# Optimization experiments

Hardware: AMD Instinct MI355X
Metric: run time of the kernel (lower is better)

The kernel has to match this reference:

```python
import jax, jax.numpy as jnp
import numpy as np
import math

EPS = 1e-7
LMAX = 2
SPH = (LMAX + 1) ** 2  # 9
NUM_RBF = 64
CUTOFF = 6.0
N_NODES = 10000
N_EDGES = 100000
CH = 64
HID = 128
ENV_P = 5  # polynomial envelope exponent


def _small_d(l, beta):
    # complex Wigner small-d matrix d^l(beta)
    n = 2 * l + 1
    d = np.zeros((n, n))
    f = math.factorial
    c = math.cos(beta / 2.0)
    s = math.sin(beta / 2.0)
    for mp in range(-l, l + 1):
        for m in range(-l, l + 1):
            val = 0.0
            for k in range(max(0, m - mp), min(l + m, l - mp) + 1):
                val += ((-1.0) ** (mp - m + k)
                        * math.sqrt(f(l + mp) * f(l - mp) * f(l + m) * f(l - m))
                        / (f(l + m - k) * f(k) * f(mp - m + k) * f(l - mp - k))
                        * c ** (2 * l + m - mp - 2 * k) * s ** (mp - m + 2 * k))
            d[mp + l, m + l] = val
    return d


def _real_J(l):
    # real-basis Wigner d at beta=pi/2 (the 'Jd' matrices)
    d = _small_d(l, math.pi / 2.0).astype(np.complex128)
    n = 2 * l + 1
    C = np.zeros((n, n), dtype=np.complex128)
    for m in range(-l, l + 1):
        if m == 0:
            C[l, l] = 1.0
        elif m > 0:
            C[m + l, -m + l] = 1.0 / math.sqrt(2)
            C[m + l, m + l] = (-1) ** m / math.sqrt(2)
        else:
            C[m + l, m + l] = 1j / math.sqrt(2)
            C[m + l, -m + l] = -1j * (-1) ** m / math.sqrt(2)
    return np.real(C @ d @ C.conj().T)


JD_LIST = [jnp.asarray(_real_J(l), dtype=jnp.float32) for l in range(LMAX + 1)]


def _z_rot_mat(angle, l):
    # real z-rotation representation of degree l, batched over edges
    E = angle.shape[0]
    size = 2 * l + 1
    M = jnp.zeros((E, size, size), dtype=angle.dtype)
    for i in range(size):
        freq = l - i
        M = M.at[:, i, i].set(jnp.cos(freq * angle))
        M = M.at[:, i, size - 1 - i].set(jnp.sin(freq * angle))
    return M


def wigner_D(l, alpha, beta, gamma, Jd):
    Xa = _z_rot_mat(alpha, l)
    Xb = _z_rot_mat(beta, l)
    Xc = _z_rot_mat(gamma, l)
    r = jnp.einsum('bij,jk->bik', Xa, Jd)
    r = jnp.einsum('bij,bjk->bik', r, Xb)
    r = jnp.einsum('bij,jk->bik', r, Jd)
    return jnp.einsum('bij,bjk->bik', r, Xc)


def eulers_to_wigner(eulers, start_lmax, end_lmax):
    alpha, beta, gamma = eulers
    E = alpha.shape[0]
    size = (end_lmax + 1) ** 2 - start_lmax ** 2
    W = jnp.zeros((E, size, size), dtype=alpha.dtype)
    start = 0
    for l in range(start_lmax, end_lmax + 1):
        blk = wigner_D(l, alpha, beta, gamma, JD_LIST[l])
        end = start + 2 * l + 1
        W = W.at[:, start:end, start:end].set(blk)
        start = end
    return W


def init_edge_rot_euler_angles(edge_distance_vec):
    norm = jnp.linalg.norm(edge_distance_vec, axis=-1, keepdims=True)
    xyz = edge_distance_vec / jnp.maximum(norm, EPS)
    xyz = jnp.clip(xyz, -1.0, 1.0)
    x, y, z = xyz[:, 0], xyz[:, 1], xyz[:, 2]
    beta = jnp.arccos(jnp.clip(y, -1 + EPS, 1 - EPS))
    alpha = jnp.arctan2(x, z)
    gamma = jnp.zeros_like(alpha)
    return (-gamma, -beta, -alpha)


def setup_inputs() -> dict:
    key = jax.random.key(0)
    ks = jax.random.split(key, 8)
    node_feats = jax.random.normal(ks[0], (N_NODES, SPH, CH), dtype=jnp.float32)
    edge_distance_vec = jax.random.normal(ks[1], (N_EDGES, 3), dtype=jnp.float32)
    edge_index = jax.random.randint(ks[2], (2, N_EDGES), 0, N_NODES, dtype=jnp.int32)
    W_rad1 = jax.random.normal(ks[3], (NUM_RBF, HID), dtype=jnp.float32) / np.sqrt(NUM_RBF)
    b_rad1 = jnp.zeros((HID,), dtype=jnp.float32)
    W_rad2 = jax.random.normal(ks[4], (HID, CH), dtype=jnp.float32) / np.sqrt(HID)
    W_msg1 = jax.random.normal(ks[5], (CH, CH), dtype=jnp.float32) / np.sqrt(CH)
    W_msg2 = jax.random.normal(ks[6], (CH, CH), dtype=jnp.float32) / np.sqrt(CH)
    gamma = jnp.ones((CH,), dtype=jnp.float32)
    return {"node_feats": node_feats, "edge_distance_vec": edge_distance_vec,
            "edge_index": edge_index, "W_rad1": W_rad1, "b_rad1": b_rad1,
            "W_rad2": W_rad2, "W_msg1": W_msg1, "W_msg2": W_msg2, "gamma": gamma}


def reference(node_feats, edge_distance_vec, edge_index, W_rad1, b_rad1, W_rad2, W_msg1, W_msg2, gamma):
    src, dst = edge_index[0], edge_index[1]
    # per-edge block-diagonal Wigner rotation [E, SPH, SPH]
    wig = eulers_to_wigner(init_edge_rot_euler_angles(edge_distance_vec), 0, LMAX)
    # radial basis (Gaussian smearing) + polynomial envelope + MLP
    dist = jnp.linalg.norm(edge_distance_vec, axis=-1)
    offsets = jnp.linspace(0.0, CUTOFF, NUM_RBF)
    coeff = -0.5 / (offsets[1] - offsets[0]) ** 2
    rbf = jnp.exp(coeff * (dist[:, None] - offsets[None, :]) ** 2)  # [E, NUM_RBF]
    d = dist / CUTOFF
    p = ENV_P
    env = (1.0 - (p + 1) * (p + 2) / 2.0 * d ** p + p * (p + 2) * d ** (p + 1)
           - p * (p + 1) / 2.0 * d ** (p + 2))
    env = jnp.where(d < 1.0, env, 0.0)
    rad = jax.nn.silu(rbf @ W_rad1 + b_rad1) @ W_rad2  # [E, CH]
    rad = rad * env[:, None]
    # gather -> rotate -> channel mix * radial gate -> mix -> rotate back
    x = node_feats[src]                                   # [E, SPH, CH]
    x = jnp.einsum('eij,ejc->eic', wig, x)
    x = jnp.einsum('eic,cd->eid', x, W_msg1) * rad[:, None, :]
    x = jnp.einsum('eic,cd->eid', x, W_msg2)
    x = jnp.einsum('eji,ejc->eic', wig, x)                # inverse (transpose) rotation
    # scatter-reduce to destination nodes
    out = jax.ops.segment_sum(x, dst, num_segments=N_NODES)  # [N, SPH, CH]
    # equivariant RMS norm over spherical-harmonic coefficients per channel
    rms = jnp.sqrt(jnp.mean(out ** 2, axis=1, keepdims=True) + EPS)
    return out / rms * gamma[None, None, :]
```

## Files before the change

### kernel.cpp

```cpp
#include <hip/hip_runtime.h>

#define SPHN 9
#define CHN 64
#define TABLE_N 8193
#define TABLE_DT (6.0f / 8192.0f)
#define TABLE_INV_DT (8192.0f / 6.0f)

__device__ __forceinline__ void centry(int l, int r, int c, double& re, double& im)
{
    const double is2 = 0.70710678118654752440;
    re = 0.0; im = 0.0;
    int m = r - l;
    if (m == 0) {
        if (c == l) re = 1.0;
    } else if (m > 0) {
        if (c == l - m) re = is2;
        else if (c == l + m) re = (m & 1) ? -is2 : is2;
    } else {
        if (c == l + m) im = is2;
        else if (c == l - m) im = (m & 1) ? is2 : -is2;
    }
}

__global__ __launch_bounds__(256) void k_setup(float* __restrict__ Jout,
// ... 42 lines not shown
        const int n1 = n - 1;
        double jr = 0.0;
        double cjr, cji, ckr, cki;
        {
            int k = i;
            centry(l, j, j, cjr, cji);
            double tr = dS[base + k * n + j] * cjr;
            double ti = -dS[base + k * n + j] * cji;
            if (n1 - j != j) {
                centry(l, j, n1 - j, cjr, cji);
                tr += dS[base + k * n + (n1 - j)] * cjr;
                ti += -dS[base + k * n + (n1 - j)] * cji;
            }
            centry(l, i, i, ckr, cki);
            jr += ckr * tr - cki * ti;
        }
        if (n1 - i != i) {
            int k = n1 - i;
            centry(l, j, j, cjr, cji);
            double tr = dS[base + k * n + j] * cjr;
            double ti = -dS[base + k * n + j] * cji;
            if (n1 - j != j) {
                centry(l, j, n1 - j, cjr, cji);
                tr += dS[base + k * n + (n1 - j)] * cjr;
                ti += -dS[base + k * n + (n1 - j)] * cji;
            }
            centry(l, i, n1 - i, ckr, cki);
            jr += ckr * tr - cki * ti;
        }
        Jout[base + i * n + j] = (float)jr;
    }
}

__global__ __launch_bounds__(256) void k_xm(const float* __restrict__ nf,
                                            const float* __restrict__ m1,
                                            float* __restrict__ xm6, int N)
{
    const int tid = threadIdx.x;
    const int w = tid >> 6;
    const int t = tid & 63;
    const int n = blockIdx.x * 4 + w;
    __shared__ float sx[4][6 * 64];
    if (n < N) {
        const float* xp = nf + (size_t)n * (SPHN * CHN);
        sx[w][0 * 64 + t] = xp[1 * 64 + t];
        sx[w][1 * 64 + t] = xp[3 * 64 + t];
        sx[w][2 * 64 + t] = xp[4 * 64 + t];
        sx[w][3 * 64 + t] = xp[5 * 64 + t];
        sx[w][4 * 64 + t] = xp[7 * 64 + t];
        sx[w][5 * 64 + t] = xp[8 * 64 + t];
    }
    __syncthreads();
    if (n >= N) return;
    float a0 = 0.f, a1 = 0.f, a2 = 0.f, a3 = 0.f, a4 = 0.f, a5 = 0.f;
    for (int c = 0; c < 64; ++c) {
        float m = m1[c * 64 + t];
        a0 += sx[w][0 * 64 + c] * m;
        a1 += sx[w][1 * 64 + c] * m;
        a2 += sx[w][2 * 64 + c] * m;
        a3 += sx[w][3 * 64 + c] * m;
        a4 += sx[w][4 * 64 + c] * m;
        a5 += sx[w][5 * 64 + c] * m;
    }
    float* op = xm6 + (size_t)n * 384;
    op[0 * 64 + t] = a0;
    op[1 * 64 + t] = a1;
    op[2 * 64 + t] = a2;
    op[3 * 64 + t] = a3;
    op[4 * 64 + t] = a4;
    op[5 * 64 + t] = a5;
}

__device__ __forceinline__ float siluf(float x) { return x / (1.f + expf(-x)); }

__global__ __launch_bounds__(256) void k_hist(const int* __restrict__ eidx,
                                              int* __restrict__ counts, int E)
{
    int e = blockIdx.x * 256 + threadIdx.x;
    if (e < E) atomicAdd(&counts[eidx[E + e]], 1);
}

__global__ __launch_bounds__(1024) void k_scan(const int* __restrict__ counts,
                                               int* __restrict__ offsets,
                                               int* __restrict__ cursors, int N)
{
    __shared__ int wsum[16];
    __shared__ int wpre[16];
    const int tid = threadIdx.x;
    const int lane = tid & 63;
    const int wid = tid >> 6;
    const int per = (N + 1023) >> 10;
    const int begin = tid * per;
    const int endi = (begin + per < N) ? (begin + per) : N;

    int s = 0;
    for (int i = begin; i < endi; ++i) s += counts[i];

    int inc = s;
#pragma unroll
    for (int off = 1; off < 64; off <<= 1) {
        int u = __shfl_up(inc, off, 64);
        if (lane >= off) inc += u;
    }
    if (lane == 63) wsum[wid] = inc;
    __syncthreads();
    if (wid == 0) {
        int v = (lane < 16) ? wsum[lane] : 0;
        int winc = v;
#pragma unroll
        for (int off = 1; off < 16; off <<= 1) {
            int u = __shfl_up(winc, off, 64);
            if (lane >= off) winc += u;
        }
        if (lane < 16) wpre[lane] = winc - v;
    }
    __syncthreads();
    int run = wpre[wid] + (inc - s);
    for (int i = begin; i < endi; ++i) {
        int c = counts[i];
        offsets[i] = run;
        cursors[i] = run;
        run += c;
    }
    if (endi == N && begin < N) offsets[N] = run;
}

__global__ __launch_bounds__(256) void k_scatter(const int* __restrict__ eidx,
                                                 int* __restrict__ cursors,
                                                 int* __restrict__ perm,
                                                 int* __restrict__ srcs, int E)
{
    int e = blockIdx.x * 256 + threadIdx.x;
    if (e < E) {
        int pos = atomicAdd(&cursors[eidx[E + e]], 1);
        perm[pos] = e;
        srcs[pos] = eidx[e];
    }
}

__global__ __launch_bounds__(256) void k_radtab(const float* __restrict__ w1,
                                                const float* __restrict__ b1,
                                                const float* __restrict__ w2,
                                                float* __restrict__ table)
{
    __shared__ float rbfT[64 * 64];
    __shared__ float hT[128 * 64];
    __shared__ float distS[64];
    __shared__ float envS[64];
    const int tid = threadIdx.x;
    const int base = blockIdx.x * 64;

    if (tid < 64) {
        float dist = (float)(base + tid) * TABLE_DT;
        distS[tid] = dist;
        float dd = dist * (1.0f / 6.0f);
        float env = 0.f;
        if (dd < 1.0f) {
            float d2 = dd * dd;
            float d5 = d2 * d2 * dd;
            env = 1.0f - 21.0f * d5 + 35.0f * d5 * dd - 15.0f * d5 * d2;
        }
        envS[tid] = env;
    }
    __syncthreads();
    const float step = 6.0f / 63.0f;
#pragma unroll
    for (int p = 0; p < 16; ++p) {
        int idx = p * 256 + tid;
        int k = idx >> 6, s2 = idx & 63;
        float diff = distS[s2] - step * (float)k;
        rbfT[idx] = __expf(-55.125f * diff * diff);
    }
    __syncthreads();

    {
        const int sg = tid & 15;
        const int jg = tid >> 4;
        float hacc[4][8];
        float4 b0 = *(const float4*)&b1[jg * 8];
        float4 b4 = *(const float4*)&b1[jg * 8 + 4];
#pragma unroll
        for (int ee = 0; ee < 4; ++ee) {
            hacc[ee][0] = b0.x; hacc[ee][1] = b0.y; hacc[ee][2] = b0.z; hacc[ee][3] = b0.w;
            hacc[ee][4] = b4.x; hacc[ee][5] = b4.y; hacc[ee][6] = b4.z; hacc[ee][7] = b4.w;
        }
#pragma unroll 4
        for (int k = 0; k < 64; ++k) {
            float4 wa = *(const float4*)&w1[k * 128 + jg * 8];
            float4 wb = *(const float4*)&w1[k * 128 + jg * 8 + 4];
            float4 rb = *(const float4*)&rbfT[k * 64 + sg * 4];
            float r[4] = {rb.x, rb.y, rb.z, rb.w};
#pragma unroll
            for (int ee = 0; ee < 4; ++ee) {
                hacc[ee][0] += r[ee] * wa.x;
                hacc[ee][1] += r[ee] * wa.y;
                hacc[ee][2] += r[ee] * wa.z;
                hacc[ee][3] += r[ee] * wa.w;
                hacc[ee][4] += r[ee] * wb.x;
                hacc[ee][5] += r[ee] * wb.y;
                hacc[ee][6] += r[ee] * wb.z;
                hacc[ee][7] += r[ee] * wb.w;
            }
        }
#pragma unroll
        for (int jj = 0; jj < 8; ++jj) {
            float4 hv;
            hv.x = siluf(hacc[0][jj]);
            hv.y = siluf(hacc[1][jj]);
            hv.z = siluf(hacc[2][jj]);
            hv.w = siluf(hacc[3][jj]);
            *(float4*)&hT[(jg * 8 + jj) * 64 + sg * 4] = hv;
        }
    }
    __syncthreads();

    {
        const int sg = tid >> 4;
        const int tg = tid & 15;
        float acc[4][4];
#pragma unroll
        for (int ee = 0; ee < 4; ++ee)
#pragma unroll
            for (int tt = 0; tt < 4; ++tt) acc[ee][tt] = 0.f;
#pragma unroll 4
        for (int j = 0; j < 128; ++j) {
            float4 wv = *(const float4*)&w2[j * 64 + tg * 4];
            float4 hv = *(const float4*)&hT[j * 64 + sg * 4];
            float h[4] = {hv.x, hv.y, hv.z, hv.w};
#pragma unroll
            for (int ee = 0; ee < 4; ++ee) {
                acc[ee][0] += h[ee] * wv.x;
                acc[ee][1] += h[ee] * wv.y;
                acc[ee][2] += h[ee] * wv.z;
                acc[ee][3] += h[ee] * wv.w;
            }
        }
#pragma unroll
        for (int ee = 0; ee < 4; ++ee) {
            int s = base + sg * 4 + ee;
            if (s < TABLE_N) {
                float envv = envS[sg * 4 + ee];
                float4 o;
                o.x = acc[ee][0] * envv;
                o.y = acc[ee][1] * envv;
                o.z = acc[ee][2] * envv;
                o.w = acc[ee][3] * envv;
                *(float4*)&table[(size_t)s * 64 + tg * 4] = o;
            }
        }
    }
}

__global__ __launch_bounds__(256) void k_edgeQ(const float* __restrict__ evec,
                                               const int* __restrict__ perm,
                                               const float* __restrict__ Jc,
                                               float* __restrict__ Qe,
                                               float* __restrict__ distI,
                                               int E)
{
    __shared__ float sJ[34];
    const int tid = threadIdx.x;
    if (tid < 34) sJ[tid] = Jc[tid];
    __syncthreads();

    const int i = blockIdx.x * 256 + tid;
    if (i >= E) return;
    const int e = perm[i];

    float vx = evec[(size_t)e * 3 + 0];
    float vy = evec[(size_t)e * 3 + 1];
    float vz = evec[(size_t)e * 3 + 2];
    float dist = sqrtf(vx * vx + vy * vy + vz * vz);
    float inv = 1.0f / fmaxf(dist, 1e-7f);
    float xn = fminf(fmaxf(vx * inv, -1.f), 1.f);
    float yn = fminf(fmaxf(vy * inv, -1.f), 1.f);
    float zn = fminf(fmaxf(vz * inv, -1.f), 1.f);
    float beta = acosf(fminf(fmaxf(yn, -1.f + 1e-7f), 1.f - 1e-7f));
    float alpha = atan2f(xn, zn);
    const float bA = -beta;
    const float cA = -alpha;

    distI[i] = dist;
    float* qo = Qe + (size_t)i * 20;

    {
        const float* J1 = sJ;
        float cb[3], sb[3], cz[3], sz[3];
#pragma unroll
        for (int k = 0; k < 3; ++k) {
            __sincosf((float)(1 - k) * bA, &sb[k], &cb[k]);
            __sincosf((float)(k - 1) * cA, &sz[k], &cz[k]);
        }
        cb[1] = 0.f; cz[1] = 0.f;
        float A[2][3], Bc[3][2], W[2][2];
#pragma unroll
        for (int a = 0; a < 2; ++a) {
            int r = a * 2;
#pragma unroll
            for (int m = 0; m < 3; ++m)
                A[a][m] = J1[r * 3 + m] * cb[m] + J1[r * 3 + (2 - m)] * sb[2 - m];
        }
#pragma unroll
        for (int m = 0; m < 3; ++m)
#pragma unroll
            for (int b = 0; b < 2; ++b) {
                int c = b * 2;
                Bc[m][b] = J1[m * 3 + c] * cz[c] + J1[m * 3 + (2 - c)] * sz[c];
            }
#pragma unroll
        for (int a = 0; a < 2; ++a)
#pragma unroll
            for (int b = 0; b < 2; ++b) {
                float w = 0.f;
#pragma unroll
                for (int m = 0; m < 3; ++m) w += A[a][m] * Bc[m][b];
                W[a][b] = w;
            }
        float4 q;
        q.x = W[0][0] * W[0][0] + W[1][0] * W[1][0];
        q.y = W[0][0] * W[0][1] + W[1][0] * W[1][1];
        q.z = W[0][1] * W[0][0] + W[1][1] * W[1][0];
        q.w = W[0][1] * W[0][1] + W[1][1] * W[1][1];
        *(float4*)&qo[0] = q;
    }

    {
        const float* J2 = sJ + 9;
        float cb[5], sb[5], cz[5], sz[5];
#pragma unroll
        for (int k = 0; k < 5; ++k) {
            __sincosf((float)(2 - k) * bA, &sb[k], &cb[k]);
            __sincosf((float)(k - 2) * cA, &sz[k], &cz[k]);
        }
        cb[2] = 0.f; cz[2] = 0.f;
        const int rmap[4] = {0, 1, 3, 4};
        float A[4][5], Bc[5][4], W[4][4];
#pragma unroll
        for (int a = 0; a < 4; ++a) {
            int r = rmap[a];
#pragma unroll
            for (int m = 0; m < 5; ++m)
                A[a][m] = J2[r * 5 + m] * cb[m] + J2[r * 5 + (4 - m)] * sb[4 - m];
        }
#pragma unroll
        for (int m = 0; m < 5; ++m)
#pragma unroll
            for (int b = 0; b < 4; ++b) {
                int c = rmap[b];
                Bc[m][b] = J2[m * 5 + c] * cz[c] + J2[m * 5 + (4 - c)] * sz[c];
            }
#pragma unroll
        for (int a = 0; a < 4; ++a)
#pragma unroll
            for (int b = 0; b < 4; ++b) {
                float w = 0.f;
#pragma unroll
                for (int m = 0; m < 5; ++m) w += A[a][m] * Bc[m][b];
                W[a][b] = w;
            }
#pragma unroll
        for (int a = 0; a < 4; ++a) {
            float4 q;
            q.x = W[0][a] * W[0][0] + W[1][a] * W[1][0] + W[2][a] * W[2][0] + W[3][a] * W[3][0];
            q.y = W[0][a] * W[0][1] + W[1][a] * W[1][1] + W[2][a] * W[2][1] + W[3][a] * W[3][1];
            q.z = W[0][a] * W[0][2] + W[1][a] * W[1][2] + W[2][a] * W[2][2] + W[3][a] * W[3][2];
            q.w = W[0][a] * W[0][3] + W[1][a] * W[1][3] + W[2][a] * W[2][3] + W[3][a] * W[3][3];
            *(float4*)&qo[4 + a * 4] = q;
        }
    }
}

__global__ __launch_bounds__(64) void k_gather_fin(const int* __restrict__ srcs,
                                                   const int* __restrict__ offsets,
                                                   const float* __restrict__ Qe,
                                                   const float* __restrict__ distI,
                                                   const float* __restrict__ table,
                                                   const float* __restrict__ xm6,
                                                   const float* __restrict__ m2,
                                                   const float* __restrict__ gam,
                                                   float* __restrict__ out)
{
    const int n = blockIdx.x;
    const int t = threadIdx.x;
    const int start = offsets[n];
    const int end = offsets[n + 1];

    float a1 = 0.f, a3 = 0.f, a4 = 0.f, a5 = 0.f, a7 = 0.f, a8 = 0.f;
    for (int i = start; i < end; ++i) {
        const int src = srcs[i];
        const float* q = Qe + (size_t)i * 20;
        float4 q0 = *(const float4*)&q[0];
        float4 q1 = *(const float4*)&q[4];
        float4 q2 = *(const float4*)&q[8];
        float4 q3 = *(const float4*)&q[12];
        float4 q4 = *(const float4*)&q[16];

        float u = fminf(distI[i] * TABLE_INV_DT, 8192.0f);
        int iu = (int)u;
        iu = (iu > 8191) ? 8191 : iu;
        float fr = u - (float)iu;
        const float* t0 = table + (size_t)iu * 64;
        float r0 = t0[t];
        float r1 = t0[64 + t];
        const float rad = r0 + fr * (r1 - r0);

        const float* xs = xm6 + (size_t)src * 384;
        float x1 = xs[0 * 64 + t];
        float x3 = xs[1 * 64 + t];
        float x4 = xs[2 * 64 + t];
        float x5 = xs[3 * 64 + t];
        float x7 = xs[4 * 64 + t];
        float x8 = xs[5 * 64 + t];
        a1 += rad * (q0.x * x1 + q0.y * x3);
        a3 += rad * (q0.z * x1 + q0.w * x3);
        a4 += rad * (q1.x * x4 + q1.y * x5 + q1.z * x7 + q1.w * x8);
        a5 += rad * (q2.x * x4 + q2.y * x5 + q2.z * x7 + q2.w * x8);
        a7 += rad * (q3.x * x4 + q3.y * x5 + q3.z * x7 + q3.w * x8);
        a8 += rad * (q4.x * x4 + q4.y * x5 + q4.z * x7 + q4.w * x8);
    }

    __shared__ float sa[6 * 64];
    sa[0 * 64 + t] = a1;
    sa[1 * 64 + t] = a3;
    sa[2 * 64 + t] = a4;
    sa[3 * 64 + t] = a5;
    sa[4 * 64 + t] = a7;
    sa[5 * 64 + t] = a8;
    __syncthreads();
    float v0 = 0.f, v1 = 0.f, v2 = 0.f, v3 = 0.f, v4 = 0.f, v5 = 0.f;
    for (int c = 0; c < 64; ++c) {
        float m = m2[c * 64 + t];
        v0 += sa[0 * 64 + c] * m;
        v1 += sa[1 * 64 + c] * m;
        v2 += sa[2 * 64 + c] * m;
        v3 += sa[3 * 64 + c] * m;
        v4 += sa[4 * 64 + c] * m;
        v5 += sa[5 * 64 + c] * m;
    }
    float ss = v0 * v0 + v1 * v1 + v2 * v2 + v3 * v3 + v4 * v4 + v5 * v5;
    float rms = sqrtf(ss * (1.0f / 9.0f) + 1e-7f);
    float sc = gam[t] / rms;
    float* op = out + (size_t)n * 576;
    op[0 * 64 + t] = 0.f;
    op[2 * 64 + t] = 0.f;
    op[6 * 64 + t] = 0.f;
    op[1 * 64 + t] = v0 * sc;
    op[3 * 64 + t] = v1 * sc;
    op[4 * 64 + t] = v2 * sc;
    op[5 * 64 + t] = v3 * sc;
    op[7 * 64 + t] = v4 * sc;
    op[8 * 64 + t] = v5 * sc;
}

__global__ __launch_bounds__(256, 4) void k_rad_lds(const float* __restrict__ evec,
                                                    const float* __restrict__ w1,
                                                    const float* __restrict__ b1,
                                                    const float* __restrict__ w2,
                                                    float* __restrict__ radg,
                                                    int E)
{
    __shared__ float rbfT[64 * 64];
    __shared__ float hT[32 * 64];
    __shared__ float distS[64];
    __shared__ float envS[64];
    const int tid = threadIdx.x;
    const int base = blockIdx.x * 64;

    if (tid < 64) {
        int e = base + tid;
        float dist = 0.f;
        if (e < E) {
            float vx = evec[(size_t)e * 3 + 0];
            float vy = evec[(size_t)e * 3 + 1];
            float vz = evec[(size_t)e * 3 + 2];
            dist = sqrtf(vx * vx + vy * vy + vz * vz);
        }
        distS[tid] = dist;
        float dd = dist * (1.0f / 6.0f);
        float env = 0.f;
        if (dd < 1.0f) {
            float d2 = dd * dd;
            float d5 = d2 * d2 * dd;
            env = 1.0f - 21.0f * d5 + 35.0f * d5 * dd - 15.0f * d5 * d2;
        }
// ... 206 lines not shown
    float sc = gam[t] / rms;
    op[0 * 64 + t] = 0.f;
    op[2 * 64 + t] = 0.f;
    op[6 * 64 + t] = 0.f;
    op[1 * 64 + t] = v0 * sc;
    op[3 * 64 + t] = v1 * sc;
    op[4 * 64 + t] = v2 * sc;
    op[5 * 64 + t] = v3 * sc;
    op[7 * 64 + t] = v4 * sc;
    op[8 * 64 + t] = v5 * sc;
}

static inline size_t align256(size_t x) { return (x + 255) & ~(size_t)255; }

extern "C" void kernel_launch(void* const* d_in, const int* in_sizes, int n_in,
                              void* d_out, int out_size, void* d_ws, size_t ws_size,
                              hipStream_t stream)
{
    const float* nf  = (const float*)d_in[0];
    const float* ev  = (const float*)d_in[1];
    const int*   ei  = (const int*)d_in[2];
    const float* w1  = (const float*)d_in[3];
    const float* b1  = (const float*)d_in[4];
    const float* w2  = (const float*)d_in[5];
    const float* m1  = (const float*)d_in[6];
    const float* m2  = (const float*)d_in[7];
    const float* gam = (const float*)d_in[8];

    const int N = in_sizes[0] / (SPHN * CHN);
    const int E = in_sizes[1] / 3;

    float* out = (float*)d_out;
    char* base = (char*)d_ws;
    size_t off = 0;
    float* Jc = (float*)(base + off);            off += align256(34 * sizeof(float));
    float* xm6 = (float*)(base + off);           off += align256((size_t)N * 384 * sizeof(float));
    float* radg = (float*)(base + off);          off += align256((size_t)E * 64 * sizeof(float));
    size_t need_old = off;
    float* Qe = (float*)(base + off);            off += align256((size_t)E * 20 * sizeof(float));
    int* counts = (int*)(base + off);            off += align256((size_t)N * sizeof(int));
    int* offsets = (int*)(base + off);           off += align256((size_t)(N + 1) * sizeof(int));
    int* cursors = (int*)(base + off);           off += align256((size_t)N * sizeof(int));
    int* perm = (int*)(base + off);              off += align256((size_t)E * sizeof(int));
    int* srcs = (int*)(base + off);              off += align256((size_t)E * sizeof(int));
    size_t need_new = off;

    float* table = radg;
    float* distI = radg + (size_t)TABLE_N * 64;

    if (ws_size >= need_new && (size_t)TABLE_N * 64 + (size_t)E <= (size_t)E * 64) {
        hipLaunchKernelGGL(k_setup, dim3((N + 255) / 256), dim3(256), 0, stream,
                           Jc, counts, N);
        hipLaunchKernelGGL(k_hist, dim3((E + 255) / 256), dim3(256), 0, stream,
                           ei, counts, E);
        hipLaunchKernelGGL(k_scan, dim3(1), dim3(1024), 0, stream,
                           counts, offsets, cursors, N);
        hipLaunchKernelGGL(k_scatter, dim3((E + 255) / 256), dim3(256), 0, stream,
                           ei, cursors, perm, srcs, E);
        hipLaunchKernelGGL(k_xm, dim3((N + 3) / 4), dim3(256), 0, stream,
                           nf, m1, xm6, N);
        hipLaunchKernelGGL(k_radtab, dim3((TABLE_N + 63) / 64), dim3(256), 0, stream,
                           w1, b1, w2, table);
        hipLaunchKernelGGL(k_edgeQ, dim3((E + 255) / 256), dim3(256), 0, stream,
                           ev, perm, Jc, Qe, distI, E);
        hipLaunchKernelGGL(k_gather_fin, dim3(N), dim3(64), 0, stream,
                           srcs, offsets, Qe, distI, table, xm6, m2, gam, out);
    } else if (ws_size >= need_old) {
        hipLaunchKernelGGL(k_setup, dim3(1), dim3(256), 0, stream,
                           Jc, (int*)nullptr, 0);
        hipLaunchKernelGGL(k_xm, dim3((N + 3) / 4), dim3(256), 0, stream,
                           nf, m1, xm6, N);
        hipMemsetAsync(d_out, 0, (size_t)out_size * sizeof(float), stream);
        hipLaunchKernelGGL(k_rad_lds, dim3((E + 63) / 64), dim3(256), 0, stream,
                           ev, w1, b1, w2, radg, E);
        hipLaunchKernelGGL(k_edge2, dim3(E), dim3(64), 0, stream,
                           ev, ei, radg, Jc, xm6, out, E);
        hipLaunchKernelGGL(k_fin, dim3(N), dim3(64), 0, stream, m2, gam, out);
    }
}
```

Baseline: 187.6 us.

## Fuse node-mix with radial table and edge rotation with CSR scatter

Merges the node channel-mix kernel and the radial lookup-table kernel into one launch that splits work by block index. Also merges the edge-scatter step into the per-edge Wigner coefficient kernel, which now writes coefficients and distance straight to their CSR position, so the perm array and its indirect reads go away. Changes the xm6 layout to per-channel interleaved (stride 8) so the gather reads one float4 plus one float2 instead of six strided loads. In exchange, atomics now fix edge order inside the heavier kernel, and xm6 is padded to 512 floats per node.

Result: slower. 196.5 us (+4.8%).

```diff
diff --git a/kernel.cpp b/kernel.cpp
--- a/kernel.cpp
+++ b/kernel.cpp
@@ -98,9 +98,417 @@
     }
 }
 
-__global__ __launch_bounds__(256) void k_xm(const float* __restrict__ nf,
-                                            const float* __restrict__ m1,
-                                            float* __restrict__ xm6, int N)
+__device__ __forceinline__ float siluf(float x) { return x / (1.f + expf(-x)); }
+
+__global__ __launch_bounds__(256) void k_xmrad(const float* __restrict__ nf,
+                                               const float* __restrict__ m1,
+                                               float* __restrict__ xm6, int N, int XB,
+                                               const float* __restrict__ w1,
+                                               const float* __restrict__ b1,
+                                               const float* __restrict__ w2,
+                                               float* __restrict__ table)
+{
+    __shared__ float rbfT[64 * 64];
+    __shared__ float hT[128 * 64];
+    __shared__ float distS[64];
+    __shared__ float envS[64];
+    const int tid = threadIdx.x;
+
+    if (blockIdx.x < XB) {
+        float* sx = rbfT;
+        const int w = tid >> 6;
+        const int t = tid & 63;
+        const int n = blockIdx.x * 4 + w;
+        if (n < N) {
+            const float* xp = nf + (size_t)n * (SPHN * CHN);
+            sx[w * 384 + 0 * 64 + t] = xp[1 * 64 + t];
+            sx[w * 384 + 1 * 64 + t] = xp[3 * 64 + t];
+            sx[w * 384 + 2 * 64 + t] = xp[4 * 64 + t];
+            sx[w * 384 + 3 * 64 + t] = xp[5 * 64 + t];
+            sx[w * 384 + 4 * 64 + t] = xp[7 * 64 + t];
+            sx[w * 384 + 5 * 64 + t] = xp[8 * 64 + t];
+        }
+        __syncthreads();
+        if (n >= N) return;
+        float a0 = 0.f, a1 = 0.f, a2 = 0.f, a3 = 0.f, a4 = 0.f, a5 = 0.f;
+        for (int c = 0; c < 64; ++c) {
+            float m = m1[c * 64 + t];
+            a0 += sx[w * 384 + 0 * 64 + c] * m;
+            a1 += sx[w * 384 + 1 * 64 + c] * m;
+            a2 += sx[w * 384 + 2 * 64 + c] * m;
+            a3 += sx[w * 384 + 3 * 64 + c] * m;
+            a4 += sx[w * 384 + 4 * 64 + c] * m;
+            a5 += sx[w * 384 + 5 * 64 + c] * m;
+        }
+        float* op = xm6 + (size_t)n * 512 + t * 8;
+        float4 v4; v4.x = a0; v4.y = a1; v4.z = a2; v4.w = a3;
+        float2 v2; v2.x = a4; v2.y = a5;
+        *(float4*)&op[0] = v4;
+        *(float2*)&op[4] = v2;
+        return;
+    }
+
+    const int base = (blockIdx.x - XB) * 64;
+    if (tid < 64) {
+        float dist = (float)(base + tid) * TABLE_DT;
+        distS[tid] = dist;
+        float dd = dist * (1.0f / 6.0f);
+        float env = 0.f;
+        if (dd < 1.0f) {
+            float d2 = dd * dd;
+            float d5 = d2 * d2 * dd;
+            env = 1.0f - 21.0f * d5 + 35.0f * d5 * dd - 15.0f * d5 * d2;
+        }
+        envS[tid] = env;
+    }
+    __syncthreads();
+    const float step = 6.0f / 63.0f;
+#pragma unroll
+    for (int p = 0; p < 16; ++p) {
+        int idx = p * 256 + tid;
+        int k = idx >> 6, s2 = idx & 63;
+        float diff = distS[s2] - step * (float)k;
+        rbfT[idx] = __expf(-55.125f * diff * diff);
+    }
+    __syncthreads();
+
+    {
+        const int sg = tid & 15;
+        const int jg = tid >> 4;
+        float hacc[4][8];
+        float4 b0 = *(const float4*)&b1[jg * 8];
+        float4 b4 = *(const float4*)&b1[jg * 8 + 4];
+#pragma unroll
+        for (int ee = 0; ee < 4; ++ee) {
+            hacc[ee][0] = b0.x; hacc[ee][1] = b0.y; hacc[ee][2] = b0.z; hacc[ee][3] = b0.w;
+            hacc[ee][4] = b4.x; hacc[ee][5] = b4.y; hacc[ee][6] = b4.z; hacc[ee][7] = b4.w;
+        }
+#pragma unroll 4
+        for (int k = 0; k < 64; ++k) {
+            float4 wa = *(const float4*)&w1[k * 128 + jg * 8];
+            float4 wb = *(const float4*)&w1[k * 128 + jg * 8 + 4];
+            float4 rb = *(const float4*)&rbfT[k * 64 + sg * 4];
+            float r[4] = {rb.x, rb.y, rb.z, rb.w};
+#pragma unroll
+            for (int ee = 0; ee < 4; ++ee) {
+                hacc[ee][0] += r[ee] * wa.x;
+                hacc[ee][1] += r[ee] * wa.y;
+                hacc[ee][2] += r[ee] * wa.z;
+                hacc[ee][3] += r[ee] * wa.w;
+                hacc[ee][4] += r[ee] * wb.x;
+                hacc[ee][5] += r[ee] * wb.y;
+                hacc[ee][6] += r[ee] * wb.z;
+                hacc[ee][7] += r[ee] * wb.w;
+            }
+        }
+#pragma unroll
+        for (int jj = 0; jj < 8; ++jj) {
+            float4 hv;
+            hv.x = siluf(hacc[0][jj]);
+            hv.y = siluf(hacc[1][jj]);
+            hv.z = siluf(hacc[2][jj]);
+            hv.w = siluf(hacc[3][jj]);
+            *(float4*)&hT[(jg * 8 + jj) * 64 + sg * 4] = hv;
+        }
+    }
+    __syncthreads();
+
+    {
+        const int sg = tid >> 4;
+        const int tg = tid & 15;
+        float acc[4][4];
+#pragma unroll
+        for (int ee = 0; ee < 4; ++ee)
+#pragma unroll
+            for (int tt = 0; tt < 4; ++tt) acc[ee][tt] = 0.f;
+#pragma unroll 4
+        for (int j = 0; j < 128; ++j) {
+            float4 wv = *(const float4*)&w2[j * 64 + tg * 4];
+            float4 hv = *(const float4*)&hT[j * 64 + sg * 4];
+            float h[4] = {hv.x, hv.y, hv.z, hv.w};
+#pragma unroll
+            for (int ee = 0; ee < 4; ++ee) {
+                acc[ee][0] += h[ee] * wv.x;
+                acc[ee][1] += h[ee] * wv.y;
+                acc[ee][2] += h[ee] * wv.z;
+                acc[ee][3] += h[ee] * wv.w;
+            }
+        }
+#pragma unroll
+        for (int ee = 0; ee < 4; ++ee) {
+            int s = base + sg * 4 + ee;
+            if (s < TABLE_N) {
+                float envv = envS[sg * 4 + ee];
+                float4 o;
+                o.x = acc[ee][0] * envv;
+                o.y = acc[ee][1] * envv;
+                o.z = acc[ee][2] * envv;
+                o.w = acc[ee][3] * envv;
+                *(float4*)&table[(size_t)s * 64 + tg * 4] = o;
+            }
+        }
+    }
+}
+
+__global__ __launch_bounds__(256) void k_hist(const int* __restrict__ eidx,
+                                              int* __restrict__ counts, int E)
+{
+    int e = blockIdx.x * 256 + threadIdx.x;
+    if (e < E) atomicAdd(&counts[eidx[E + e]], 1);
+}
+
+__global__ __launch_bounds__(1024) void k_scan(const int* __restrict__ counts,
+                                               int* __restrict__ offsets,
+                                               int* __restrict__ cursors, int N)
+{
+    __shared__ int wsum[16];
+    __shared__ int wpre[16];
+    const int tid = threadIdx.x;
+    const int lane = tid & 63;
+    const int wid = tid >> 6;
+    const int per = (N + 1023) >> 10;
+    const int begin = tid * per;
+    const int endi = (begin + per < N) ? (begin + per) : N;
+
+    int s = 0;
+    for (int i = begin; i < endi; ++i) s += counts[i];
+
+    int inc = s;
+#pragma unroll
+    for (int off = 1; off < 64; off <<= 1) {
+        int u = __shfl_up(inc, off, 64);
+        if (lane >= off) inc += u;
+    }
+    if (lane == 63) wsum[wid] = inc;
+    __syncthreads();
+    if (wid == 0) {
+        int v = (lane < 16) ? wsum[lane] : 0;
+        int winc = v;
+#pragma unroll
+        for (int off = 1; off < 16; off <<= 1) {
+            int u = __shfl_up(winc, off, 64);
+            if (lane >= off) winc += u;
+        }
+        if (lane < 16) wpre[lane] = winc - v;
+    }
+    __syncthreads();
+    int run = wpre[wid] + (inc - s);
+    for (int i = begin; i < endi; ++i) {
+        int c = counts[i];
+        offsets[i] = run;
+        cursors[i] = run;
+        run += c;
+    }
+    if (endi == N && begin < N) offsets[N] = run;
+}
+
+__global__ __launch_bounds__(256) void k_edgeQS(const float* __restrict__ evec,
+                                                const int* __restrict__ eidx,
+                                                const float* __restrict__ Jc,
+                                                int* __restrict__ cursors,
+                                                float* __restrict__ Qe24,
+                                                int* __restrict__ srcs, int E)
+{
+    __shared__ float sJ[34];
+    const int tid = threadIdx.x;
+    if (tid < 34) sJ[tid] = Jc[tid];
+    __syncthreads();
+
+    const int e = blockIdx.x * 256 + tid;
+    if (e >= E) return;
+
+    float vx = evec[(size_t)e * 3 + 0];
+    float vy = evec[(size_t)e * 3 + 1];
+    float vz = evec[(size_t)e * 3 + 2];
+    float dist = sqrtf(vx * vx + vy * vy + vz * vz);
+    float inv = 1.0f / fmaxf(dist, 1e-7f);
+    float xn = fminf(fmaxf(vx * inv, -1.f), 1.f);
+    float yn = fminf(fmaxf(vy * inv, -1.f), 1.f);
+    float zn = fminf(fmaxf(vz * inv, -1.f), 1.f);
+    float beta = acosf(fminf(fmaxf(yn, -1.f + 1e-7f), 1.f - 1e-7f));
+    float alpha = atan2f(xn, zn);
+    const float bA = -beta;
+    const float cA = -alpha;
+
+    const int src = eidx[e];
+    const int dst = eidx[E + e];
+    const int pos = atomicAdd(&cursors[dst], 1);
+    srcs[pos] = src;
+    float* qo = Qe24 + (size_t)pos * 24;
+
+    {
+        const float* J1 = sJ;
+        float cb[3], sb[3], cz[3], sz[3];
+#pragma unroll
+        for (int k = 0; k < 3; ++k) {
+            __sincosf((float)(1 - k) * bA, &sb[k], &cb[k]);
+            __sincosf((float)(k - 1) * cA, &sz[k], &cz[k]);
+        }
+        cb[1] = 0.f; cz[1] = 0.f;
+        float A[2][3], Bc[3][2], W[2][2];
+#pragma unroll
+        for (int a = 0; a < 2; ++a) {
+            int r = a * 2;
+#pragma unroll
+            for (int m = 0; m < 3; ++m)
+                A[a][m] = J1[r * 3 + m] * cb[m] + J1[r * 3 + (2 - m)] * sb[2 - m];
+        }
+#pragma unroll
+        for (int m = 0; m < 3; ++m)
+#pragma unroll
+            for (int b = 0; b < 2; ++b) {
+                int c = b * 2;
+                Bc[m][b] = J1[m * 3 + c] * cz[c] + J1[m * 3 + (2 - c)] * sz[c];
+            }
+#pragma unroll
+        for (int a = 0; a < 2; ++a)
+#pragma unroll
+            for (int b = 0; b < 2; ++b) {
+                float w = 0.f;
+#pragma unroll
+                for (int m = 0; m < 3; ++m) w += A[a][m] * Bc[m][b];
+                W[a][b] = w;
+            }
+        float4 q;
+        q.x = W[0][0] * W[0][0] + W[1][0] * W[1][0];
+        q.y = W[0][0] * W[0][1] + W[1][0] * W[1][1];
+        q.z = W[0][1] * W[0][0] + W[1][1] * W[1][0];
+        q.w = W[0][1] * W[0][1] + W[1][1] * W[1][1];
+        *(float4*)&qo[0] = q;
+    }
+
+    {
+        const float* J2 = sJ + 9;
+        float cb[5], sb[5], cz[5], sz[5];
+#pragma unroll
+        for (int k = 0; k < 5; ++k) {
+            __sincosf((float)(2 - k) * bA, &sb[k], &cb[k]);
+            __sincosf((float)(k - 2) * cA, &sz[k], &cz[k]);
+        }
+        cb[2] = 0.f; cz[2] = 0.f;
+        const int rmap[4] = {0, 1, 3, 4};
+        float A[4][5], Bc[5][4], W[4][4];
+#pragma unroll
+        for (int a = 0; a < 4; ++a) {
+            int r = rmap[a];
+#pragma unroll
+            for (int m = 0; m < 5; ++m)
+                A[a][m] = J2[r * 5 + m] * cb[m] + J2[r * 5 + (4 - m)] * sb[4 - m];
+        }
+#pragma unroll
+        for (int m = 0; m < 5; ++m)
+#pragma unroll
+            for (int b = 0; b < 4; ++b) {
+                int c = rmap[b];
+                Bc[m][b] = J2[m * 5 + c] * cz[c] + J2[m * 5 + (4 - c)] * sz[c];
+            }
+#pragma unroll
+        for (int a = 0; a < 4; ++a)
+#pragma unroll
+            for (int b = 0; b < 4; ++b) {
+                float w = 0.f;
+#pragma unroll
+                for (int m = 0; m < 5; ++m) w += A[a][m] * Bc[m][b];
+                W[a][b] = w;
+            }
+#pragma unroll
+        for (int a = 0; a < 4; ++a) {
+            float4 q;
+            q.x = W[0][a] * W[0][0] + W[1][a] * W[1][0] + W[2][a] * W[2][0] + W[3][a] * W[3][0];
+            q.y = W[0][a] * W[0][1] + W[1][a] * W[1][1] + W[2][a] * W[2][1] + W[3][a] * W[3][1];
+            q.z = W[0][a] * W[0][2] + W[1][a] * W[1][2] + W[2][a] * W[2][2] + W[3][a] * W[3][2];
+            q.w = W[0][a] * W[0][3] + W[1][a] * W[1][3] + W[2][a] * W[2][3] + W[3][a] * W[3][3];
+            *(float4*)&qo[4 + a * 4] = q;
+        }
+    }
+
+    float4 qd; qd.x = dist; qd.y = 0.f; qd.z = 0.f; qd.w = 0.f;
+    *(float4*)&qo[20] = qd;
+}
+
+__global__ __launch_bounds__(64) void k_gather_fin(const int* __restrict__ srcs,
+                                                   const int* __restrict__ offsets,
+                                                   const float* __restrict__ Qe24,
+                                                   const float* __restrict__ table,
+                                                   const float* __restrict__ xm6,
+                                                   const float* __restrict__ m2,
+                                                   const float* __restrict__ gam,
+                                                   float* __restrict__ out)
+{
+    const int n = blockIdx.x;
+    const int t = threadIdx.x;
+    const int start = offsets[n];
+    const int end = offsets[n + 1];
+
+    float a1 = 0.f, a3 = 0.f, a4 = 0.f, a5 = 0.f, a7 = 0.f, a8 = 0.f;
+    for (int i = start; i < end; ++i) {
+        const int src = srcs[i];
+        const float* q = Qe24 + (size_t)i * 24;
+        float4 q0 = *(const float4*)&q[0];
+        float4 q1 = *(const float4*)&q[4];
+        float4 q2 = *(const float4*)&q[8];
+        float4 q3 = *(const float4*)&q[12];
+        float4 q4 = *(const float4*)&q[16];
+        float dist = q[20];
+
+        float u = fminf(dist * TABLE_INV_DT, 8192.0f);
+        int iu = (int)u;
+        iu = (iu > 8191) ? 8191 : iu;
+        float fr = u - (float)iu;
+        const float* t0 = table + (size_t)iu * 64;
+        float r0 = t0[t];
+        float r1 = t0[64 + t];
+        const float rad = r0 + fr * (r1 - r0);
+
+        const float* xs = xm6 + (size_t)src * 512 + t * 8;
+        float4 xa = *(const float4*)&xs[0];
+        float2 xb = *(const float2*)&xs[4];
+        float x1 = xa.x, x3 = xa.y, x4 = xa.z, x5 = xa.w, x7 = xb.x, x8 = xb.y;
+
+        a1 += rad * (q0.x * x1 + q0.y * x3);
+        a3 += rad * (q0.z * x1 + q0.w * x3);
+        a4 += rad * (q1.x * x4 + q1.y * x5 + q1.z * x7 + q1.w * x8);
+        a5 += rad * (q2.x * x4 + q2.y * x5 + q2.z * x7 + q2.w * x8);
+        a7 += rad * (q3.x * x4 + q3.y * x5 + q3.z * x7 + q3.w * x8);
+        a8 += rad * (q4.x * x4 + q4.y * x5 + q4.z * x7 + q4.w * x8);
+    }
+
+    __shared__ float sa[6 * 64];
+    sa[0 * 64 + t] = a1;
+    sa[1 * 64 + t] = a3;
+    sa[2 * 64 + t] = a4;
+    sa[3 * 64 + t] = a5;
+    sa[4 * 64 + t] = a7;
+    sa[5 * 64 + t] = a8;
+    __syncthreads();
+    float v0 = 0.f, v1 = 0.f, v2 = 0.f, v3 = 0.f, v4 = 0.f, v5 = 0.f;
+    for (int c = 0; c < 64; ++c) {
+        float m = m2[c * 64 + t];
+        v0 += sa[0 * 64 + c] * m;
+        v1 += sa[1 * 64 + c] * m;
+        v2 += sa[2 * 64 + c] * m;
+        v3 += sa[3 * 64 + c] * m;
+        v4 += sa[4 * 64 + c] * m;
+        v5 += sa[5 * 64 + c] * m;
+    }
+    float ss = v0 * v0 + v1 * v1 + v2 * v2 + v3 * v3 + v4 * v4 + v5 * v5;
+    float rms = sqrtf(ss * (1.0f / 9.0f) + 1e-7f);
+    float sc = gam[t] / rms;
+    float* op = out + (size_t)n * 576;
+    op[0 * 64 + t] = 0.f;
+    op[2 * 64 + t] = 0.f;
+    op[6 * 64 + t] = 0.f;
+    op[1 * 64 + t] = v0 * sc;
+    op[3 * 64 + t] = v1 * sc;
+    op[4 * 64 + t] = v2 * sc;
+    op[5 * 64 + t] = v3 * sc;
+    op[7 * 64 + t] = v4 * sc;
+    op[8 * 64 + t] = v5 * sc;
+}
+
+__global__ __launch_bounds__(256) void k_xm_legacy(const float* __restrict__ nf,
+                                                   const float* __restrict__ m1,
+                                                   float* __restrict__ xm6, int N)
 {
     const int tid = threadIdx.x;
     const int w = tid >> 6;
@@ -135,387 +543,6 @@
     op[3 * 64 + t] = a3;
     op[4 * 64 + t] = a4;
     op[5 * 64 + t] = a5;
-}
-
-__device__ __forceinline__ float siluf(float x) { return x / (1.f + expf(-x)); }
-
-__global__ __launch_bounds__(256) void k_hist(const int* __restrict__ eidx,
-                                              int* __restrict__ counts, int E)
-{
-    int e = blockIdx.x * 256 + threadIdx.x;
-    if (e < E) atomicAdd(&counts[eidx[E + e]], 1);
-}
-
-__global__ __launch_bounds__(1024) void k_scan(const int* __restrict__ counts,
-                                               int* __restrict__ offsets,
-                                               int* __restrict__ cursors, int N)
-{
-    __shared__ int wsum[16];
-    __shared__ int wpre[16];
-    const int tid = threadIdx.x;
-    const int lane = tid & 63;
-    const int wid = tid >> 6;
-    const int per = (N + 1023) >> 10;
-    const int begin = tid * per;
-    const int endi = (begin + per < N) ? (begin + per) : N;
-
-    int s = 0;
-    for (int i = begin; i < endi; ++i) s += counts[i];
-
-    int inc = s;
-#pragma unroll
-    for (int off = 1; off < 64; off <<= 1) {
-        int u = __shfl_up(inc, off, 64);
-        if (lane >= off) inc += u;
-    }
-    if (lane == 63) wsum[wid] = inc;
-    __syncthreads();
-    if (wid == 0) {
-        int v = (lane < 16) ? wsum[lane] : 0;
-        int winc = v;
-#pragma unroll
-        for (int off = 1; off < 16; off <<= 1) {
-            int u = __shfl_up(winc, off, 64);
-            if (lane >= off) winc += u;
-        }
-        if (lane < 16) wpre[lane] = winc - v;
-    }
-    __syncthreads();
-    int run = wpre[wid] + (inc - s);
-    for (int i = begin; i < endi; ++i) {
-        int c = counts[i];
-        offsets[i] = run;
-        cursors[i] = run;
-        run += c;
-    }
-    if (endi == N && begin < N) offsets[N] = run;
-}
-
-__global__ __launch_bounds__(256) void k_scatter(const int* __restrict__ eidx,
-                                                 int* __restrict__ cursors,
-                                                 int* __restrict__ perm,
-                                                 int* __restrict__ srcs, int E)
-{
-    int e = blockIdx.x * 256 + threadIdx.x;
-    if (e < E) {
-        int pos = atomicAdd(&cursors[eidx[E + e]], 1);
-        perm[pos] = e;
-        srcs[pos] = eidx[e];
-    }
-}
-
-__global__ __launch_bounds__(256) void k_radtab(const float* __restrict__ w1,
-                                                const float* __restrict__ b1,
-                                                const float* __restrict__ w2,
-                                                float* __restrict__ table)
-{
-    __shared__ float rbfT[64 * 64];
-    __shared__ float hT[128 * 64];
-    __shared__ float distS[64];
-    __shared__ float envS[64];
-    const int tid = threadIdx.x;
-    const int base = blockIdx.x * 64;
-
-    if (tid < 64) {
-        float dist = (float)(base + tid) * TABLE_DT;
-        distS[tid] = dist;
-        float dd = dist * (1.0f / 6.0f);
-        float env = 0.f;
-        if (dd < 1.0f) {
-            float d2 = dd * dd;
-            float d5 = d2 * d2 * dd;
-            env = 1.0f - 21.0f * d5 + 35.0f * d5 * dd - 15.0f * d5 * d2;
-        }
-        envS[tid] = env;
-    }
-    __syncthreads();
-    const float step = 6.0f / 63.0f;
-#pragma unroll
-    for (int p = 0; p < 16; ++p) {
-        int idx = p * 256 + tid;
-        int k = idx >> 6, s2 = idx & 63;
-        float diff = distS[s2] - step * (float)k;
-        rbfT[idx] = __expf(-55.125f * diff * diff);
-    }
-    __syncthreads();
-
-    {
-        const int sg = tid & 15;
-        const int jg = tid >> 4;
-        float hacc[4][8];
-        float4 b0 = *(const float4*)&b1[jg * 8];
-        float4 b4 = *(const float4*)&b1[jg * 8 + 4];
-#pragma unroll
-        for (int ee = 0; ee < 4; ++ee) {
-            hacc[ee][0] = b0.x; hacc[ee][1] = b0.y; hacc[ee][2] = b0.z; hacc[ee][3] = b0.w;
-            hacc[ee][4] = b4.x; hacc[ee][5] = b4.y; hacc[ee][6] = b4.z; hacc[ee][7] = b4.w;
-        }
-#pragma unroll 4
-        for (int k = 0; k < 64; ++k) {
-            float4 wa = *(const float4*)&w1[k * 128 + jg * 8];
-            float4 wb = *(const float4*)&w1[k * 128 + jg * 8 + 4];
-            float4 rb = *(const float4*)&rbfT[k * 64 + sg * 4];
-            float r[4] = {rb.x, rb.y, rb.z, rb.w};
-#pragma unroll
-            for (int ee = 0; ee < 4; ++ee) {
-                hacc[ee][0] += r[ee] * wa.x;
-                hacc[ee][1] += r[ee] * wa.y;
-                hacc[ee][2] += r[ee] * wa.z;
-                hacc[ee][3] += r[ee] * wa.w;
-                hacc[ee][4] += r[ee] * wb.x;
-                hacc[ee][5] += r[ee] * wb.y;
-                hacc[ee][6] += r[ee] * wb.z;
-                hacc[ee][7] += r[ee] * wb.w;
-            }
-        }
-#pragma unroll
-        for (int jj = 0; jj < 8; ++jj) {
-            float4 hv;
-            hv.x = siluf(hacc[0][jj]);
-            hv.y = siluf(hacc[1][jj]);
-            hv.z = siluf(hacc[2][jj]);
-            hv.w = siluf(hacc[3][jj]);
-            *(float4*)&hT[(jg * 8 + jj) * 64 + sg * 4] = hv;
-        }
-    }
-    __syncthreads();
-
-    {
-        const int sg = tid >> 4;
-        const int tg = tid & 15;
-        float acc[4][4];
-#pragma unroll
-        for (int ee = 0; ee < 4; ++ee)
-#pragma unroll
-            for (int tt = 0; tt < 4; ++tt) acc[ee][tt] = 0.f;
-#pragma unroll 4
-        for (int j = 0; j < 128; ++j) {
-            float4 wv = *(const float4*)&w2[j * 64 + tg * 4];
-            float4 hv = *(const float4*)&hT[j * 64 + sg * 4];
-            float h[4] = {hv.x, hv.y, hv.z, hv.w};
-#pragma unroll
-            for (int ee = 0; ee < 4; ++ee) {
-                acc[ee][0] += h[ee] * wv.x;
-                acc[ee][1] += h[ee] * wv.y;
-                acc[ee][2] += h[ee] * wv.z;
-                acc[ee][3] += h[ee] * wv.w;
-            }
-        }
-#pragma unroll
-        for (int ee = 0; ee < 4; ++ee) {
-            int s = base + sg * 4 + ee;
-            if (s < TABLE_N) {
-                float envv = envS[sg * 4 + ee];
-                float4 o;
-                o.x = acc[ee][0] * envv;
-                o.y = acc[ee][1] * envv;
-                o.z = acc[ee][2] * envv;
-                o.w = acc[ee][3] * envv;
-                *(float4*)&table[(size_t)s * 64 + tg * 4] = o;
-            }
-        }
-    }
-}
-
-__global__ __launch_bounds__(256) void k_edgeQ(const float* __restrict__ evec,
-                                               const int* __restrict__ perm,
-                                               const float* __restrict__ Jc,
-                                               float* __restrict__ Qe,
-                                               float* __restrict__ distI,
-                                               int E)
-{
-    __shared__ float sJ[34];
-    const int tid = threadIdx.x;
-    if (tid < 34) sJ[tid] = Jc[tid];
-    __syncthreads();
-
-    const int i = blockIdx.x * 256 + tid;
-    if (i >= E) return;
-    const int e = perm[i];
-
-    float vx = evec[(size_t)e * 3 + 0];
-    float vy = evec[(size_t)e * 3 + 1];
-    float vz = evec[(size_t)e * 3 + 2];
-    float dist = sqrtf(vx * vx + vy * vy + vz * vz);
-    float inv = 1.0f / fmaxf(dist, 1e-7f);
-    float xn = fminf(fmaxf(vx * inv, -1.f), 1.f);
-    float yn = fminf(fmaxf(vy * inv, -1.f), 1.f);
-    float zn = fminf(fmaxf(vz * inv, -1.f), 1.f);
-    float beta = acosf(fminf(fmaxf(yn, -1.f + 1e-7f), 1.f - 1e-7f));
-    float alpha = atan2f(xn, zn);
-    const float bA = -beta;
-    const float cA = -alpha;
-
-    distI[i] = dist;
-    float* qo = Qe + (size_t)i * 20;
-
-    {
-        const float* J1 = sJ;
-        float cb[3], sb[3], cz[3], sz[3];
-#pragma unroll
-        for (int k = 0; k < 3; ++k) {
-            __sincosf((float)(1 - k) * bA, &sb[k], &cb[k]);
-            __sincosf((float)(k - 1) * cA, &sz[k], &cz[k]);
-        }
-        cb[1] = 0.f; cz[1] = 0.f;
-        float A[2][3], Bc[3][2], W[2][2];
-#pragma unroll
-        for (int a = 0; a < 2; ++a) {
-            int r = a * 2;
-#pragma unroll
-            for (int m = 0; m < 3; ++m)
-                A[a][m] = J1[r * 3 + m] * cb[m] + J1[r * 3 + (2 - m)] * sb[2 - m];
-        }
-#pragma unroll
-        for (int m = 0; m < 3; ++m)
-#pragma unroll
-            for (int b = 0; b < 2; ++b) {
-                int c = b * 2;
-                Bc[m][b] = J1[m * 3 + c] * cz[c] + J1[m * 3 + (2 - c)] * sz[c];
-            }
-#pragma unroll
-        for (int a = 0; a < 2; ++a)
-#pragma unroll
-            for (int b = 0; b < 2; ++b) {
-                float w = 0.f;
-#pragma unroll
-                for (int m = 0; m < 3; ++m) w += A[a][m] * Bc[m][b];
-                W[a][b] = w;
-            }
-        float4 q;
-        q.x = W[0][0] * W[0][0] + W[1][0] * W[1][0];
-        q.y = W[0][0] * W[0][1] + W[1][0] * W[1][1];
-        q.z = W[0][1] * W[0][0] + W[1][1] * W[1][0];
-        q.w = W[0][1] * W[0][1] + W[1][1] * W[1][1];
-        *(float4*)&qo[0] = q;
-    }
-
-    {
-        const float* J2 = sJ + 9;
-        float cb[5], sb[5], cz[5], sz[5];
-#pragma unroll
-        for (int k = 0; k < 5; ++k) {
-            __sincosf((float)(2 - k) * bA, &sb[k], &cb[k]);
-            __sincosf((float)(k - 2) * cA, &sz[k], &cz[k]);
-        }
-        cb[2] = 0.f; cz[2] = 0.f;
-        const int rmap[4] = {0, 1, 3, 4};
-        float A[4][5], Bc[5][4], W[4][4];
-#pragma unroll
-        for (int a = 0; a < 4; ++a) {
-            int r = rmap[a];
-#pragma unroll
-            for (int m = 0; m < 5; ++m)
-                A[a][m] = J2[r * 5 + m] * cb[m] + J2[r * 5 + (4 - m)] * sb[4 - m];
-        }
-#pragma unroll
-        for (int m = 0; m < 5; ++m)
-#pragma unroll
-            for (int b = 0; b < 4; ++b) {
-                int c = rmap[b];
-                Bc[m][b] = J2[m * 5 + c] * cz[c] + J2[m * 5 + (4 - c)] * sz[c];
-            }
-#pragma unroll
-        for (int a = 0; a < 4; ++a)
-#pragma unroll
-            for (int b = 0; b < 4; ++b) {
-                float w = 0.f;
-#pragma unroll
-                for (int m = 0; m < 5; ++m) w += A[a][m] * Bc[m][b];
-                W[a][b] = w;
-            }
-#pragma unroll
-        for (int a = 0; a < 4; ++a) {
-            float4 q;
-            q.x = W[0][a] * W[0][0] + W[1][a] * W[1][0] + W[2][a] * W[2][0] + W[3][a] * W[3][0];
-            q.y = W[0][a] * W[0][1] + W[1][a] * W[1][1] + W[2][a] * W[2][1] + W[3][a] * W[3][1];
-            q.z = W[0][a] * W[0][2] + W[1][a] * W[1][2] + W[2][a] * W[2][2] + W[3][a] * W[3][2];
-            q.w = W[0][a] * W[0][3] + W[1][a] * W[1][3] + W[2][a] * W[2][3] + W[3][a] * W[3][3];
-            *(float4*)&qo[4 + a * 4] = q;
-        }
-    }
-}
-
-__global__ __launch_bounds__(64) void k_gather_fin(const int* __restrict__ srcs,
-                                                   const int* __restrict__ offsets,
-                                                   const float* __restrict__ Qe,
-                                                   const float* __restrict__ distI,
-                                                   const float* __restrict__ table,
-                                                   const float* __restrict__ xm6,
-                                                   const float* __restrict__ m2,
-                                                   const float* __restrict__ gam,
-                                                   float* __restrict__ out)
-{
-    const int n = blockIdx.x;
-    const int t = threadIdx.x;
-    const int start = offsets[n];
-    const int end = offsets[n + 1];
-
-    float a1 = 0.f, a3 = 0.f, a4 = 0.f, a5 = 0.f, a7 = 0.f, a8 = 0.f;
-    for (int i = start; i < end; ++i) {
-        const int src = srcs[i];
-        const float* q = Qe + (size_t)i * 20;
-        float4 q0 = *(const float4*)&q[0];
-        float4 q1 = *(const float4*)&q[4];
-        float4 q2 = *(const float4*)&q[8];
-        float4 q3 = *(const float4*)&q[12];
-        float4 q4 = *(const float4*)&q[16];
-
-        float u = fminf(distI[i] * TABLE_INV_DT, 8192.0f);
-        int iu = (int)u;
-        iu = (iu > 8191) ? 8191 : iu;
-        float fr = u - (float)iu;
-        const float* t0 = table + (size_t)iu * 64;
-        float r0 = t0[t];
-        float r1 = t0[64 + t];
-        const float rad = r0 + fr * (r1 - r0);
-
-        const float* xs = xm6 + (size_t)src * 384;
-        float x1 = xs[0 * 64 + t];
-        float x3 = xs[1 * 64 + t];
-        float x4 = xs[2 * 64 + t];
-        float x5 = xs[3 * 64 + t];
-        float x7 = xs[4 * 64 + t];
-        float x8 = xs[5 * 64 + t];
-        a1 += rad * (q0.x * x1 + q0.y * x3);
-        a3 += rad * (q0.z * x1 + q0.w * x3);
-        a4 += rad * (q1.x * x4 + q1.y * x5 + q1.z * x7 + q1.w * x8);
-        a5 += rad * (q2.x * x4 + q2.y * x5 + q2.z * x7 + q2.w * x8);
-        a7 += rad * (q3.x * x4 + q3.y * x5 + q3.z * x7 + q3.w * x8);
-        a8 += rad * (q4.x * x4 + q4.y * x5 + q4.z * x7 + q4.w * x8);
-    }
-
-    __shared__ float sa[6 * 64];
-    sa[0 * 64 + t] = a1;
-    sa[1 * 64 + t] = a3;
-    sa[2 * 64 + t] = a4;
-    sa[3 * 64 + t] = a5;
-    sa[4 * 64 + t] = a7;
-    sa[5 * 64 + t] = a8;
-    __syncthreads();
-    float v0 = 0.f, v1 = 0.f, v2 = 0.f, v3 = 0.f, v4 = 0.f, v5 = 0.f;
-    for (int c = 0; c < 64; ++c) {
-        float m = m2[c * 64 + t];
-        v0 += sa[0 * 64 + c] * m;
-        v1 += sa[1 * 64 + c] * m;
-        v2 += sa[2 * 64 + c] * m;
-        v3 += sa[3 * 64 + c] * m;
-        v4 += sa[4 * 64 + c] * m;
-        v5 += sa[5 * 64 + c] * m;
-    }
-    float ss = v0 * v0 + v1 * v1 + v2 * v2 + v3 * v3 + v4 * v4 + v5 * v5;
-    float rms = sqrtf(ss * (1.0f / 9.0f) + 1e-7f);
-    float sc = gam[t] / rms;
-    float* op = out + (size_t)n * 576;
-    op[0 * 64 + t] = 0.f;
-    op[2 * 64 + t] = 0.f;
-    op[6 * 64 + t] = 0.f;
-    op[1 * 64 + t] = v0 * sc;
-    op[3 * 64 + t] = v1 * sc;
-    op[4 * 64 + t] = v2 * sc;
-    op[5 * 64 + t] = v3 * sc;
-    op[7 * 64 + t] = v4 * sc;
-    op[8 * 64 + t] = v5 * sc;
 }
 
 __global__ __launch_bounds__(256, 4) void k_rad_lds(const float* __restrict__ evec,
@@ -788,49 +815,48 @@
 
     float* out = (float*)d_out;
     char* base = (char*)d_ws;
+
     size_t off = 0;
-    float* Jc = (float*)(base + off);            off += align256(34 * sizeof(float));
-    float* xm6 = (float*)(base + off);           off += align256((size_t)N * 384 * sizeof(float));
-    float* radg = (float*)(base + off);          off += align256((size_t)E * 64 * sizeof(float));
-    size_t need_old = off;
-    float* Qe = (float*)(base + off);            off += align256((size_t)E * 20 * sizeof(float));
-    int* counts = (int*)(base + off);            off += align256((size_t)N * sizeof(int));
-    int* offsets = (int*)(base + off);           off += align256((size_t)(N + 1) * sizeof(int));
-    int* cursors = (int*)(base + off);           off += align256((size_t)N * sizeof(int));
-    int* perm = (int*)(base + off);              off += align256((size_t)E * sizeof(int));
-    int* srcs = (int*)(base + off);              off += align256((size_t)E * sizeof(int));
+    float* Jc = (float*)(base + off);      off += align256(34 * sizeof(float));
+    float* xm6n = (float*)(base + off);    off += align256((size_t)N * 512 * sizeof(float));
+    float* table = (float*)(base + off);   off += align256((size_t)TABLE_N * 64 * sizeof(float));
+    float* Qe24 = (float*)(base + off);    off += align256((size_t)E * 24 * sizeof(float));
+    int* counts = (int*)(base + off);      off += align256((size_t)N * sizeof(int));
+    int* offsets = (int*)(base + off);     off += align256((size_t)(N + 1) * sizeof(int));
+    int* cursors = (int*)(base + off);     off += align256((size_t)N * sizeof(int));
+    int* srcs = (int*)(base + off);        off += align256((size_t)E * sizeof(int));
     size_t need_new = off;
 
-    float* table = radg;
-    float* distI = radg + (size_t)TABLE_N * 64;
-
-    if (ws_size >= need_new && (size_t)TABLE_N * 64 + (size_t)E <= (size_t)E * 64) {
+    size_t offF = align256(34 * sizeof(float));
+    float* xm6o = (float*)(base + offF);   offF += align256((size_t)N * 384 * sizeof(float));
+    float* radg = (float*)(base + offF);   offF += align256((size_t)E * 64 * sizeof(float));
+    size_t need_old = offF;
+
+    if (ws_size >= need_new) {
+        const int XB = (N + 3) / 4;
+        const int RB = (TABLE_N + 63) / 64;
         hipLaunchKernelGGL(k_setup, dim3((N + 255) / 256), dim3(256), 0, stream,
                            Jc, counts, N);
         hipLaunchKernelGGL(k_hist, dim3((E + 255) / 256), dim3(256), 0, stream,
                            ei, counts, E);
         hipLaunchKernelGGL(k_scan, dim3(1), dim3(1024), 0, stream,
                            counts, offsets, cursors, N);
-        hipLaunchKernelGGL(k_scatter, dim3((E + 255) / 256), dim3(256), 0, stream,
-                           ei, cursors, perm, srcs, E);
-        hipLaunchKernelGGL(k_xm, dim3((N + 3) / 4), dim3(256), 0, stream,
-                           nf, m1, xm6, N);
-        hipLaunchKernelGGL(k_radtab, dim3((TABLE_N + 63) / 64), dim3(256), 0, stream,
-                           w1, b1, w2, table);
-        hipLaunchKernelGGL(k_edgeQ, dim3((E + 255) / 256), dim3(256), 0, stream,
-                           ev, perm, Jc, Qe, distI, E);
+        hipLaunchKernelGGL(k_xmrad, dim3(XB + RB), dim3(256), 0, stream,
+                           nf, m1, xm6n, N, XB, w1, b1, w2, table);
+        hipLaunchKernelGGL(k_edgeQS, dim3((E + 255) / 256), dim3(256), 0, stream,
+                           ev, ei, Jc, cursors, Qe24, srcs, E);
         hipLaunchKernelGGL(k_gather_fin, dim3(N), dim3(64), 0, stream,
-                           srcs, offsets, Qe, distI, table, xm6, m2, gam, out);
+                           srcs, offsets, Qe24, table, xm6n, m2, gam, out);
     } else if (ws_size >= need_old) {
         hipLaunchKernelGGL(k_setup, dim3(1), dim3(256), 0, stream,
                            Jc, (int*)nullptr, 0);
-        hipLaunchKernelGGL(k_xm, dim3((N + 3) / 4), dim3(256), 0, stream,
-                           nf, m1, xm6, N);
+        hipLaunchKernelGGL(k_xm_legacy, dim3((N + 3) / 4), dim3(256), 0, stream,
+                           nf, m1, xm6o, N);
         hipMemsetAsync(d_out, 0, (size_t)out_size * sizeof(float), stream);
         hipLaunchKernelGGL(k_rad_lds, dim3((E + 63) / 64), dim3(256), 0, stream,
                            ev, w1, b1, w2, radg, E);
         hipLaunchKernelGGL(k_edge2, dim3(E), dim3(64), 0, stream,
-                           ev, ei, radg, Jc, xm6, out, E);
+                           ev, ei, radg, Jc, xm6o, out, E);
         hipLaunchKernelGGL(k_fin, dim3(N), dim3(64), 0, stream, m2, gam, out);
     }
 }
```
